# Kernel optimization log

Hardware: AMD Instinct MI355X
Metric: run time of the kernel (lower is better)

The kernel has to match this reference:

```python
import jax, jax.numpy as jnp
from jax import lax
import numpy as np
import math

IN_CH = 256
SCALES = [128, 256, 512]
ASPECT = [0.5, 1.0, 2.0]
NUM_A = len(SCALES) * len(ASPECT)  # 9
PRENMS_TOPK = 2000
RPN_TOPK = 1000
NMS_TH = 0.7
MIN_SIZE = 16.0
IMG_H = IMG_W = 1600
FEAT_H = FEAT_W = 200
BBOX_CLIP = math.log(1000.0 / 16.0)  # standard dw/dh clamp in box decoding


def setup_inputs() -> dict:
    key = jax.random.key(0)
    ks = jax.random.split(key, 6)
    image = jax.random.normal(ks[0], (1, 3, IMG_H, IMG_W), jnp.float32)
    feat = jax.random.normal(ks[1], (1, IN_CH, FEAT_H, FEAT_W), jnp.float32)
    # params init per init_weights(): normal(std=0.01), zero bias
    conv_w = jax.random.normal(ks[2], (IN_CH, IN_CH, 3, 3), jnp.float32) * 0.01
    conv_b = jnp.zeros((IN_CH,), jnp.float32)
    cls_w = jax.random.normal(ks[3], (NUM_A, IN_CH, 1, 1), jnp.float32) * 0.01
    cls_b = jnp.zeros((NUM_A,), jnp.float32)
    reg_w = jax.random.normal(ks[4], (NUM_A * 4, IN_CH, 1, 1), jnp.float32) * 0.01
    reg_b = jnp.zeros((NUM_A * 4,), jnp.float32)
    return dict(image=image, feat=feat, conv_w=conv_w, conv_b=conv_b,
                cls_w=cls_w, cls_b=cls_b, reg_w=reg_w, reg_b=reg_b)


def _conv(x, w, b, pad):
    y = lax.conv_general_dilated(x, w, (1, 1), [(pad, pad), (pad, pad)],
                                 dimension_numbers=('NCHW', 'OIHW', 'NCHW'))
    return y + b[None, :, None, None]


def _generate_anchors(img_hw, feat_hw):
    # static (numpy) anchor grid, faithful to generate_anchors_
    gh, gw = feat_hw
    ih, iw = img_hw
    sh, sw = ih // gh, iw // gw
    scales = np.array(SCALES, np.float32)
    ar = np.array(ASPECT, np.float32)
    hr = np.sqrt(ar)
    wr = 1.0 / hr
    ws = (wr[:, None] * scales[None, :]).reshape(-1)
    hs = (hr[:, None] * scales[None, :]).reshape(-1)
    base = np.round(np.stack([-ws, -hs, ws, hs], axis=1) / 2.0)  # (A,4)
    sx = np.arange(gw, dtype=np.float32) * sw
    sy = np.arange(gh, dtype=np.float32) * sh
    yy, xx = np.meshgrid(sy, sx, indexing='ij')
    xx = xx.reshape(-1)
    yy = yy.reshape(-1)
    shifts = np.stack([xx, yy, xx, yy], axis=1)  # (H*W,4)
    anchors = (shifts[:, None, :] + base[None, :, :]).reshape(-1, 4)
    return jnp.asarray(anchors, jnp.float32)


def _apply_deltas(anchors, deltas):
    w = anchors[:, 2] - anchors[:, 0]
    h = anchors[:, 3] - anchors[:, 1]
    cx = anchors[:, 0] + 0.5 * w
    cy = anchors[:, 1] + 0.5 * h
    dx, dy = deltas[:, 0], deltas[:, 1]
    dw = jnp.minimum(deltas[:, 2], BBOX_CLIP)
    dh = jnp.minimum(deltas[:, 3], BBOX_CLIP)
    pcx = dx * w + cx
    pcy = dy * h + cy
    pw = jnp.exp(dw) * w
    ph = jnp.exp(dh) * h
    return jnp.stack([pcx - 0.5 * pw, pcy - 0.5 * ph,
                      pcx + 0.5 * pw, pcy + 0.5 * ph], axis=1)


def _nms_keep(boxes, valid, thresh):
    # boxes sorted by descending score; greedy NMS via dense IoU matrix
    K = boxes.shape[0]
    area = (boxes[:, 2] - boxes[:, 0]) * (boxes[:, 3] - boxes[:, 1])
    lt = jnp.maximum(boxes[:, None, :2], boxes[None, :, :2])
    rb = jnp.minimum(boxes[:, None, 2:], boxes[None, :, 2:])
    wh = jnp.maximum(rb - lt, 0.0)
    inter = wh[..., 0] * wh[..., 1]
    iou = inter / (area[:, None] + area[None, :] - inter + 1e-9)
    idx = jnp.arange(K)

    def body(i, keep):
        sup = (iou[i] > thresh) & keep[i] & (idx > i)
        return keep & (~sup)

    return lax.fori_loop(0, K, body, valid)


def reference(image, feat, conv_w, conv_b, cls_w, cls_b, reg_w, reg_b):
    H, W = feat.shape[-2], feat.shape[-1]
    x = jax.nn.relu(_conv(feat, conv_w, conv_b, 1))          # (1,C,H,W)
    cls = _conv(x, cls_w, cls_b, 0)                          # (1,A,H,W)
    scores = cls.transpose(0, 2, 3, 1).reshape(-1)           # (H*W*A,)
    reg = _conv(x, reg_w, reg_b, 0)                          # (1,4A,H,W)
    deltas = reg.reshape(1, NUM_A, 4, H, W).transpose(0, 3, 4, 1, 2).reshape(-1, 4)
    anchors = _generate_anchors((image.shape[-2], image.shape[-1]), (H, W))
    proposals = _apply_deltas(anchors, lax.stop_gradient(deltas))  # .detach() in source

    s = jax.nn.sigmoid(scores)
    topv, topi = lax.top_k(s, PRENMS_TOPK)                   # sorted descending
    p = proposals[topi]
    ih = jnp.float32(image.shape[-2])
    iw = jnp.float32(image.shape[-1])
    p = jnp.stack([jnp.clip(p[:, 0], 0.0, iw), jnp.clip(p[:, 1], 0.0, ih),
                   jnp.clip(p[:, 2], 0.0, iw), jnp.clip(p[:, 3], 0.0, ih)], axis=1)
    valid = ((p[:, 2] - p[:, 0]) >= MIN_SIZE) & ((p[:, 3] - p[:, 1]) >= MIN_SIZE)
    sc = jnp.where(valid, topv, -1.0)                        # invalid -> score -1 (masked out)
    order = jnp.argsort(-sc)
    b = p[order]
    sc = sc[order]
    v = valid[order]
    keep = _nms_keep(b, v, NMS_TH)
    final = jnp.where(keep, sc, -1.0)
    fi = jnp.argsort(-final)[:RPN_TOPK]                      # post-NMS sort + topk
    sel = final[fi]
    out_boxes = jnp.where(sel[:, None] > 0.0, b[fi], 0.0)
    out_scores = jnp.where(sel > 0.0, sel, 0.0)
    return out_boxes, out_scores
```

## Files before the change

kernel.cpp:

```cpp
#include <hip/hip_runtime.h>
#include <math.h>

#define FH 200
#define FW 200
#define HW 40000
#define NUM_A 9
#define NANCH 360000
#define PRE_K 2000
#define OUT_K 1000
#define IMG_SZ 1600.0f
#define MIN_SZ 16.0f
#define NMS_TH 0.7f
#define BBOX_CLIP_F 4.135166556742356f

#define OFF_HIST   ((size_t)0)
#define OFF_STATE  ((size_t)1024)
#define OFF_CAND   ((size_t)1088)
#define OFF_BOXS   ((size_t)33856)
#define OFF_SCS    ((size_t)65856)
#define OFF_MASK   ((size_t)73856)
#define OFF_DIAG   ((size_t)585856)
#define OFF_AWH    ((size_t)602240)
#define OFF_AWM    ((size_t)1781888)
#define OFF_AWL    ((size_t)2961536)
#define OFF_HWH    ((size_t)4141184)
#define OFF_HWM    ((size_t)4165760)
#define OFF_HWL    ((size_t)4190336)
#define OFF_LOGIT  ((size_t)4214912)
#define OFF_PH     ((size_t)18614912)
#define OFF_PM     ((size_t)39094912)
#define OFF_PL     ((size_t)59574912)
#define OFF_PROP   ((size_t)18614912)
#define OFF_SCORE  ((size_t)24374912)

typedef __attribute__((ext_vector_type(8))) short short8;
typedef __attribute__((ext_vector_type(4))) float floatx4;
#define MFMA16(a, b, c) __builtin_amdgcn_mfma_f32_16x16x32_bf16(a, b, c, 0, 0, 0)

__device__ __forceinline__ unsigned short rne_bf16(float v) {
  unsigned int bb = __float_as_uint(v);
  return (unsigned short)((bb + 0x7FFFu + ((bb >> 16) & 1u)) >> 16);
}

__device__ __forceinline__ void split3(float v, unsigned short& h,
                                       unsigned short& m, unsigned short& l) {
  h = rne_bf16(v);
  float r1 = v - __uint_as_float(((unsigned int)h) << 16);
  m = rne_bf16(r1);
  float r2 = r1 - __uint_as_float(((unsigned int)m) << 16);
  l = rne_bf16(r2);
}

__global__ __launch_bounds__(256) void prep_all(
    const float* __restrict__ feat, const float* __restrict__ w,
    const float* __restrict__ cls_w, const float* __restrict__ reg_w,
    unsigned short* __restrict__ Ph, unsigned short* __restrict__ Pm,
    unsigned short* __restrict__ Pl, uint4* __restrict__ AW_h,
    uint4* __restrict__ AW_m, uint4* __restrict__ AW_l,
    uint4* __restrict__ HwF_h, uint4* __restrict__ HwF_m,
    uint4* __restrict__ HwF_l) {
  int bx = blockIdx.x;
  int t = threadIdx.x;
  if (bx < 1256) {
    int cib = bx & 7;
    int px = (bx >> 3) * 256 + t;
    if (px >= HW) return;
    unsigned short h[32], m[32], l[32];
#pragma unroll
    for (int ci = 0; ci < 32; ++ci)
      split3(feat[(size_t)(cib * 32 + ci) * HW + px], h[ci], m[ci], l[ci]);
    size_t base = ((size_t)cib * HW + px) * 32;
    uint4* dh = (uint4*)(Ph + base);
    uint4* dm = (uint4*)(Pm + base);
    uint4* dl = (uint4*)(Pl + base);
#pragma unroll
    for (int k = 0; k < 4; ++k) {
      uint4 vh, vm, vl;
      vh.x = h[k * 8 + 0] | (h[k * 8 + 1] << 16);
      vh.y = h[k * 8 + 2] | (h[k * 8 + 3] << 16);
      vh.z = h[k * 8 + 4] | (h[k * 8 + 5] << 16);
      vh.w = h[k * 8 + 6] | (h[k * 8 + 7] << 16);
      vm.x = m[k * 8 + 0] | (m[k * 8 + 1] << 16);
      vm.y = m[k * 8 + 2] | (m[k * 8 + 3] << 16);
      vm.z = m[k * 8 + 4] | (m[k * 8 + 5] << 16);
      vm.w = m[k * 8 + 6] | (m[k * 8 + 7] << 16);
      vl.x = l[k * 8 + 0] | (l[k * 8 + 1] << 16);
      vl.y = l[k * 8 + 2] | (l[k * 8 + 3] << 16);
      vl.z = l[k * 8 + 4] | (l[k * 8 + 5] << 16);
      vl.w = l[k * 8 + 6] | (l[k * 8 + 7] << 16);
      dh[k] = vh; dm[k] = vm; dl[k] = vl;
    }
    return;
  }
  int gid = (bx - 1256) * 256 + t;
  unsigned short h[8], m[8], l[8];
  if (gid < 73728) {
    int L = gid & 63;
    int idx = gid >> 6;
    int cib = idx & 7;
    int tmp = idx >> 3;
    int tap = tmp % 9;
    int ctg = tmp / 9;
    int co = ctg * 16 + (L & 15);
    int ci0 = cib * 32 + (L >> 4) * 8;
#pragma unroll
    for (int j = 0; j < 8; ++j)
      split3(w[(size_t)co * 2304 + (ci0 + j) * 9 + tap], h[j], m[j], l[j]);
    uint4 vh, vm, vl;
    vh.x = h[0] | (h[1] << 16); vh.y = h[2] | (h[3] << 16);
    vh.z = h[4] | (h[5] << 16); vh.w = h[6] | (h[7] << 16);
    vm.x = m[0] | (m[1] << 16); vm.y = m[2] | (m[3] << 16);
    vm.z = m[4] | (m[5] << 16); vm.w = m[6] | (m[7] << 16);
    vl.x = l[0] | (l[1] << 16); vl.y = l[2] | (l[3] << 16);
    vl.z = l[4] | (l[5] << 16); vl.w = l[6] | (l[7] << 16);
    AW_h[gid] = vh; AW_m[gid] = vm; AW_l[gid] = vl;
  } else if (gid < 73728 + 1536) {
    int g2 = gid - 73728;
    int L = g2 & 63;
    int idx = g2 >> 6;
    int kb = idx & 7;
    int mt = idx >> 3;
    int mm = mt * 16 + (L & 15);
    int co0 = kb * 32 + (L >> 4) * 8;
#pragma unroll
    for (int j = 0; j < 8; ++j) {
      float v = 0.f;
      if (mm < 9) v = cls_w[mm * 256 + co0 + j];
      else if (mm < 45) v = reg_w[(mm - 9) * 256 + co0 + j];
      split3(v, h[j], m[j], l[j]);
    }
    uint4 vh, vm, vl;
    vh.x = h[0] | (h[1] << 16); vh.y = h[2] | (h[3] << 16);
    vh.z = h[4] | (h[5] << 16); vh.w = h[6] | (h[7] << 16);
    vm.x = m[0] | (m[1] << 16); vm.y = m[2] | (m[3] << 16);
    vm.z = m[4] | (m[5] << 16); vm.w = m[6] | (m[7] << 16);
    vl.x = l[0] | (l[1] << 16); vl.y = l[2] | (l[3] << 16);
    vl.z = l[4] | (l[5] << 16); vl.w = l[6] | (l[7] << 16);
    HwF_h[g2] = vh; HwF_m[g2] = vm; HwF_l[g2] = vl;
  }
}

__global__ __launch_bounds__(256) void conv_mfma(
    const unsigned short* __restrict__ Ph, const unsigned short* __restrict__ Pm,
    const unsigned short* __restrict__ Pl, const uint4* __restrict__ AW_h,
    const uint4* __restrict__ AW_m, const uint4* __restrict__ AW_l,
    const uint4* __restrict__ HwF_h, const uint4* __restrict__ HwF_m,
    const uint4* __restrict__ HwF_l, const float* __restrict__ bias,
    float* __restrict__ logits) {
  __shared__ alignas(16) unsigned short smem[26112];
  const int t = threadIdx.x;
  const int L = t & 63, wv = t >> 6;
  const int q = L >> 4, nl = L & 15;
  const int w0 = blockIdx.x * 16;
  const int h0 = blockIdx.y * 8;
  const int cb = blockIdx.z;

  floatx4 acc[2][8];
#pragma unroll
  for (int ct = 0; ct < 2; ++ct)
#pragma unroll
    for (int r = 0; r < 8; ++r) acc[ct][r] = (floatx4)0.f;

  unsigned short* flh = smem;
  unsigned short* flm = smem + 7200;
  unsigned short* fll = smem + 14400;

  for (int cib = 0; cib < 8; ++cib) {
    __syncthreads();
#pragma unroll
    for (int j = 0; j < 9; ++j) {
      const int p = j / 3;
      const int c = (j % 3) * 256 + t;
      if (c < 720) {
        int rr = (int)((unsigned)c / 72u);
        int rem = c - rr * 72;
        int cc = rem >> 2, q16 = rem & 3;
        int gr = h0 - 1 + rr, gc = w0 - 1 + cc;
        uint4 v; v.x = v.y = v.z = v.w = 0u;
        if ((unsigned)gr < (unsigned)FH && (unsigned)gc < (unsigned)FW) {
          const unsigned short* pp = (p == 0) ? Ph : (p == 1) ? Pm : Pl;
          v = *(const uint4*)(pp +
                ((size_t)(cib * HW + gr * FW + gc) * 32 + q16 * 8));
        }
        *(uint4*)(smem + p * 7200 + rr * 720 + cc * 40 + q16 * 8) = v;
      }
    }
    __syncthreads();
    __builtin_amdgcn_s_setprio(1);
    const int ctg0 = cb * 8 + wv * 2;
    for (int kh = 0; kh < 3; ++kh) {
      for (int kw = 0; kw < 3; ++kw) {
        const int tap = kh * 3 + kw;
        const int abase = ((ctg0 * 9 + tap) * 8 + cib) * 64 + L;
        const int abase1 = abase + 9 * 8 * 64;
        short8 ah0 = ((const short8*)AW_h)[abase];
        short8 am0 = ((const short8*)AW_m)[abase];
        short8 al0 = ((const short8*)AW_l)[abase];
        short8 ah1 = ((const short8*)AW_h)[abase1];
        short8 am1 = ((const short8*)AW_m)[abase1];
        short8 al1 = ((const short8*)AW_l)[abase1];
        const int cbase = (nl + kw) * 40 + q * 8;
#pragma unroll
        for (int r = 0; r < 8; ++r) {
          const int off = (r + kh) * 720 + cbase;
          short8 bh = *(const short8*)(flh + off);
          short8 bm = *(const short8*)(flm + off);
          short8 bl = *(const short8*)(fll + off);
          acc[0][r] = MFMA16(ah0, bh, acc[0][r]);
          acc[0][r] = MFMA16(ah0, bm, acc[0][r]);
          acc[0][r] = MFMA16(am0, bh, acc[0][r]);
          acc[0][r] = MFMA16(ah0, bl, acc[0][r]);
          acc[0][r] = MFMA16(am0, bm, acc[0][r]);
          acc[0][r] = MFMA16(al0, bh, acc[0][r]);
          acc[1][r] = MFMA16(ah1, bh, acc[1][r]);
          acc[1][r] = MFMA16(ah1, bm, acc[1][r]);
          acc[1][r] = MFMA16(am1, bh, acc[1][r]);
          acc[1][r] = MFMA16(ah1, bl, acc[1][r]);
          acc[1][r] = MFMA16(am1, bm, acc[1][r]);
          acc[1][r] = MFMA16(al1, bh, acc[1][r]);
        }
      }
    }
    __builtin_amdgcn_s_setprio(0);
  }

  float bv[2][4];
#pragma unroll
  for (int ct = 0; ct < 2; ++ct)
#pragma unroll
    for (int i = 0; i < 4; ++i)
      bv[ct][i] = bias[cb * 128 + (wv * 2 + ct) * 16 + q * 4 + i];

  unsigned short* xlh = smem;
  unsigned short* xlm = smem + 8704;
  unsigned short* xll = smem + 17408;

  for (int hp = 0; hp < 2; ++hp) {
    __syncthreads();
#pragma unroll
    for (int ct = 0; ct < 2; ++ct) {
#pragma unroll
      for (int rr = 0; rr < 4; ++rr) {
        int r = hp * 4 + rr;
        unsigned short xh[4], xm[4], xl_[4];
#pragma unroll
        for (int i = 0; i < 4; ++i) {
          float xv = fmaxf(acc[ct][r][i] + bv[ct][i], 0.f);
          split3(xv, xh[i], xm[i], xl_[i]);
        }
        int px_l = rr * 16 + nl;
        int co_l = (wv * 2 + ct) * 16 + q * 4;
        uint2 ph, pm, pl;
        ph.x = xh[0] | (xh[1] << 16); ph.y = xh[2] | (xh[3] << 16);
        pm.x = xm[0] | (xm[1] << 16); pm.y = xm[2] | (xm[3] << 16);
        pl.x = xl_[0] | (xl_[1] << 16); pl.y = xl_[2] | (xl_[3] << 16);
        *(uint2*)(xlh + px_l * 136 + co_l) = ph;
        *(uint2*)(xlm + px_l * 136 + co_l) = pm;
        *(uint2*)(xll + px_l * 136 + co_l) = pl;
      }
    }
    __syncthreads();
    floatx4 ha[3];
#pragma unroll
    for (int mt = 0; mt < 3; ++mt) ha[mt] = (floatx4)0.f;
    for (int ks = 0; ks < 4; ++ks) {
      const int off = (wv * 16 + nl) * 136 + ks * 32 + q * 8;
      short8 bh = *(const short8*)(xlh + off);
      short8 bm = *(const short8*)(xlm + off);
      short8 bl = *(const short8*)(xll + off);
#pragma unroll
      for (int mt = 0; mt < 3; ++mt) {
        const int hb = (mt * 8 + cb * 4 + ks) * 64 + L;
        short8 hh = ((const short8*)HwF_h)[hb];
        short8 hm = ((const short8*)HwF_m)[hb];
        short8 hl = ((const short8*)HwF_l)[hb];
        ha[mt] = MFMA16(hh, bh, ha[mt]);
        ha[mt] = MFMA16(hh, bm, ha[mt]);
        ha[mt] = MFMA16(hm, bh, ha[mt]);
        ha[mt] = MFMA16(hh, bl, ha[mt]);
        ha[mt] = MFMA16(hm, bm, ha[mt]);
        ha[mt] = MFMA16(hl, bh, ha[mt]);
      }
    }
    int gr = h0 + hp * 4 + wv;
    int gc = w0 + nl;
    if (gc < FW) {
      float* lp = logits + ((size_t)cb * HW + (size_t)(gr * FW + gc)) * 45;
#pragma unroll
      for (int mt = 0; mt < 3; ++mt)
#pragma unroll
        for (int i = 0; i < 4; ++i) {
          int head = mt * 16 + q * 4 + i;
          if (head < 45) lp[head] = ha[mt][i];
        }
    }
  }
}

__global__ __launch_bounds__(256) void finalize_kernel(
    const float* __restrict__ logits, const float* __restrict__ cls_b,
    const float* __restrict__ reg_b, float* __restrict__ prop,
    float* __restrict__ score, unsigned int* __restrict__ hist) {
  __shared__ unsigned int hsh[256];
  int t = threadIdx.x;
  hsh[t] = 0u;
  __syncthreads();
  int px = blockIdx.x * 256 + t;
  if (px < HW) {
    float A[45];
    const float* lpA = logits + (size_t)px * 45;
    const float* lpB = logits + (size_t)HW * 45 + (size_t)px * 45;
#pragma unroll
    for (int i = 0; i < 45; ++i) A[i] = lpA[i] + lpB[i];
    const float scv[3] = {128.f, 256.f, 512.f};
    const float arv[3] = {0.5f, 1.f, 2.f};
    float sx = (float)(px % FW) * 8.0f;
    float sy = (float)(px / FW) * 8.0f;
#pragma unroll
    for (int a = 0; a < NUM_A; ++a) {
      int ai = a / 3, si = a % 3;
      float hr = sqrtf(arv[ai]);
      float wr = 1.0f / hr;
      float rw = nearbyintf(wr * scv[si] * 0.5f);
      float rh = nearbyintf(hr * scv[si] * 0.5f);
      float ax0 = sx - rw, ay0 = sy - rh, ax1 = sx + rw, ay1 = sy + rh;
      float aw = ax1 - ax0, ah = ay1 - ay0;
      float cx = ax0 + 0.5f * aw, cy = ay0 + 0.5f * ah;
      float dx = A[9 + a * 4 + 0] + reg_b[a * 4 + 0];
      float dy = A[9 + a * 4 + 1] + reg_b[a * 4 + 1];
      float dw = fminf(A[9 + a * 4 + 2] + reg_b[a * 4 + 2], BBOX_CLIP_F);
      float dh = fminf(A[9 + a * 4 + 3] + reg_b[a * 4 + 3], BBOX_CLIP_F);
      float pcx = dx * aw + cx;
      float pcy = dy * ah + cy;
      float pw = expf(dw) * aw;
      float ph = expf(dh) * ah;
      size_t base = (size_t)(px * NUM_A + a) * 4;
      prop[base + 0] = pcx - 0.5f * pw;
      prop[base + 1] = pcy - 0.5f * ph;
      prop[base + 2] = pcx + 0.5f * pw;
      prop[base + 3] = pcy + 0.5f * ph;
      float lg = A[a] + cls_b[a];
      float sv = 1.0f / (1.0f + expf(-lg));
      score[px * NUM_A + a] = sv;
      atomicAdd(&hsh[__float_as_uint(sv) >> 24], 1u);
    }
  }
  __syncthreads();
  if (hsh[t]) atomicAdd(&hist[t], hsh[t]);
}

__global__ __launch_bounds__(256) void hist_kernel(
    const float* __restrict__ score, unsigned int* __restrict__ hist,
    const unsigned int* __restrict__ state, int pass) {
  __shared__ unsigned int h[256];
  int t = threadIdx.x;
  h[t] = 0;
  __syncthreads();
  unsigned int prefix = state[0];
  int shift = 24 - 8 * pass;
  for (int i = blockIdx.x * 256 + t; i < NANCH; i += gridDim.x * 256) {
    unsigned int key = __float_as_uint(score[i]);
    bool m = ((key >> (32 - 8 * pass)) == prefix);
    if (m) atomicAdd(&h[(key >> shift) & 255u], 1u);
  }
  __syncthreads();
  if (h[t]) atomicAdd(&hist[t], h[t]);
}

__global__ __launch_bounds__(256) void scan_kernel(
    unsigned int* __restrict__ hist, unsigned int* __restrict__ state, int pass) {
  __shared__ unsigned int s0[256], s1[256];
  int t = threadIdx.x;
  unsigned int hv = hist[t];
  hist[t] = 0u;
  s0[t] = hv;
  __syncthreads();
  unsigned int* A = s0;
  unsigned int* B = s1;
  for (int off = 1; off < 256; off <<= 1) {
    B[t] = A[t] + ((t + off < 256) ? A[t + off] : 0u);
    __syncthreads();
    unsigned int* tmp = A; A = B; B = tmp;
  }
  unsigned int prefix = (pass == 0) ? 0u : state[0];
  unsigned int rem = (pass == 0) ? (unsigned)PRE_K : state[1];
  unsigned int suf = A[t];
  unsigned int sufn = (t < 255) ? A[t + 1] : 0u;
  if (suf >= rem && sufn < rem) {
    state[0] = (prefix << 8) | (unsigned int)t;
    state[1] = rem - sufn;
  }
}

__global__ __launch_bounds__(256) void collect_kernel(
    const float* __restrict__ score, unsigned int* __restrict__ state,
    unsigned long long* __restrict__ cand) {
  unsigned int T = state[0];
  for (int i = blockIdx.x * 256 + threadIdx.x; i < NANCH; i += gridDim.x * 256) {
    unsigned int key = __float_as_uint(score[i]);
    if (key >= T) {
      unsigned int pos = atomicAdd(&state[4], 1u);
      if (pos < 4096u)
        cand[pos] = ((unsigned long long)key << 32) |
                    (unsigned long long)(~(unsigned int)i);
    }
  }
}

__global__ __launch_bounds__(1024) void sort_gather(
    const unsigned long long* __restrict__ cand,
    const unsigned int* __restrict__ state, const float* __restrict__ prop,
    const float* __restrict__ score, float* __restrict__ boxes_s,
    float* __restrict__ sc_s) {
  __shared__ unsigned long long sk[4096];
  int t = threadIdx.x;
  unsigned int cnt = state[4];
  if (cnt > 4096u) cnt = 4096u;
  for (int e = t; e < 4096; e += 1024) sk[e] = (e < (int)cnt) ? cand[e] : 0ull;
  __syncthreads();
  for (int k = 2; k <= 4096; k <<= 1) {
    for (int j = k >> 1; j > 0; j >>= 1) {
      for (int i = t; i < 4096; i += 1024) {
        int l = i ^ j;
        if (l > i) {
          unsigned long long a = sk[i], bb = sk[l];
          bool up = ((i & k) == 0);
          bool sw = up ? (a < bb) : (a > bb);
          if (sw) { sk[i] = bb; sk[l] = a; }
        }
      }
      __syncthreads();
    }
  }
  float bx[2][4];
  float sc2[2] = {-1.f, -1.f};
  bool valid2[2] = {false, false};
#pragma unroll
  for (int s = 0; s < 2; ++s) {
    int i = t + s * 1024;
    bx[s][0] = bx[s][1] = bx[s][2] = bx[s][3] = 0.f;
    if (i < PRE_K) {
      unsigned long long v = sk[i];
      unsigned int idx = ~(unsigned int)(v & 0xFFFFFFFFull);
      float4 p = *(const float4*)(prop + (size_t)idx * 4);
      float x0 = fminf(fmaxf(p.x, 0.f), IMG_SZ);
      float y0 = fminf(fmaxf(p.y, 0.f), IMG_SZ);
      float x1 = fminf(fmaxf(p.z, 0.f), IMG_SZ);
      float y1 = fminf(fmaxf(p.w, 0.f), IMG_SZ);
      bool valid = (x1 - x0 >= MIN_SZ) && (y1 - y0 >= MIN_SZ);
      bx[s][0] = x0; bx[s][1] = y0; bx[s][2] = x1; bx[s][3] = y1;
      valid2[s] = valid;
      sc2[s] = valid ? score[idx] : -1.0f;
    }
  }
  __syncthreads();
  int* A = (int*)sk;
  int* B = A + 2048;
#pragma unroll
  for (int s = 0; s < 2; ++s) {
    int i = t + s * 1024;
    A[i] = (i < PRE_K && valid2[s]) ? 1 : 0;
  }
  __syncthreads();
  for (int off = 1; off < 2048; off <<= 1) {
#pragma unroll
    for (int s = 0; s < 2; ++s) {
      int i = t + s * 1024;
      B[i] = A[i] + ((i >= off) ? A[i - off] : 0);
    }
    __syncthreads();
    int* tmp = A; A = B; B = tmp;
  }
  int total = A[2047];
#pragma unroll
  for (int s = 0; s < 2; ++s) {
    int i = t + s * 1024;
    if (i < PRE_K) {
      int inc = A[i];
      int pos = valid2[s] ? (inc - 1) : (total + (i - inc));
      boxes_s[pos * 4 + 0] = bx[s][0];
      boxes_s[pos * 4 + 1] = bx[s][1];
      boxes_s[pos * 4 + 2] = bx[s][2];
      boxes_s[pos * 4 + 3] = bx[s][3];
      sc_s[pos] = sc2[s];
    }
  }
}

__global__ __launch_bounds__(64) void iou_kernel(
    const float* __restrict__ boxes_s, unsigned long long* __restrict__ mask,
    unsigned long long* __restrict__ diag) {
  int bi = blockIdx.y, bj = blockIdx.x;
  int t = threadIdx.x;
  __shared__ float4 cb[64];
  int jc = bj * 64 + t;
  float4 z; z.x = z.y = z.z = z.w = 0.f;
  cb[t] = (jc < PRE_K) ? *(const float4*)(boxes_s + (size_t)jc * 4) : z;
  __syncthreads();
  int i = bi * 64 + t;
  if (i >= PRE_K) return;
  float4 a = *(const float4*)(boxes_s + (size_t)i * 4);
  float areaA = (a.z - a.x) * (a.w - a.y);
  unsigned long long bits = 0ull;
  for (int jj = 0; jj < 64; ++jj) {
    int j = bj * 64 + jj;
    if (j < PRE_K && j > i) {
      float4 b = cb[jj];
      float areaB = (b.z - b.x) * (b.w - b.y);
      float ltx = fmaxf(a.x, b.x), lty = fmaxf(a.y, b.y);
      float rbx = fminf(a.z, b.z), rby = fminf(a.w, b.w);
      float w = fmaxf(rbx - ltx, 0.f), h = fmaxf(rby - lty, 0.f);
      float inter = w * h;
      float iou = inter / (areaA + areaB - inter + 1e-9f);
      if (iou > NMS_TH) bits |= (1ull << jj);
    }
  }
  mask[(size_t)i * 32 + bj] = bits;
  if (bi == bj) diag[i] = bits;
}

__global__ __launch_bounds__(256) void nms_out_kernel(
    const float* __restrict__ boxes_s, const float* __restrict__ sc_s,
    const unsigned long long* __restrict__ mask,
    const unsigned long long* __restrict__ diag, float* __restrict__ out) {
  int t = threadIdx.x;
  for (int e = t; e < (OUT_K * 4 + OUT_K); e += 256) out[e] = 0.f;
  __shared__ unsigned long long keepw[32];
  if (t < 64) {
    unsigned long long removed = 0ull;
    if (t < 32) {
      keepw[t] = 0ull;
#pragma unroll
      for (int k = 0; k < 64; ++k) {
        int idx = t * 64 + k;
        if (idx >= PRE_K || sc_s[idx] < 0.f) removed |= (1ull << k);
      }
    }
    const int w = t & 31;
    const int half = t >> 5;
    unsigned int kept = 0;
    for (int b = 0; b < 32; ++b) {
      unsigned long long d = diag[b * 64 + t];
      unsigned long long dead = __shfl(removed, b);
      unsigned long long alive = 0ull;
#pragma unroll
      for (int k = 0; k < 64; ++k) {
        unsigned long long dk = __shfl(d, k);
        if (!((dead >> k) & 1ull)) {
          alive |= (1ull << k);
          dead |= dk;
        }
      }
      if (t == 0) keepw[b] = alive;
      kept += (unsigned)__popcll(alive);
      if (kept >= (unsigned)OUT_K || b == 31) break;
      unsigned long long am = alive;
      const long long rb = (long long)b * 64;
      while (am) {
        int k0 = __ffsll(am) - 1; am &= am - 1;
        int k1 = k0, k2 = k0, k3 = k0, k4 = k0, k5 = k0, k6 = k0, k7 = k0;
        if (am) { k1 = __ffsll(am) - 1; am &= am - 1; }
        if (am) { k2 = __ffsll(am) - 1; am &= am - 1; }
        if (am) { k3 = __ffsll(am) - 1; am &= am - 1; }
        if (am) { k4 = __ffsll(am) - 1; am &= am - 1; }
        if (am) { k5 = __ffsll(am) - 1; am &= am - 1; }
        if (am) { k6 = __ffsll(am) - 1; am &= am - 1; }
        if (am) { k7 = __ffsll(am) - 1; am &= am - 1; }
        unsigned long long v0 = mask[(size_t)(rb + (half ? k1 : k0)) * 32 + w];
        unsigned long long v1 = mask[(size_t)(rb + (half ? k3 : k2)) * 32 + w];
        unsigned long long v2 = mask[(size_t)(rb + (half ? k5 : k4)) * 32 + w];
        unsigned long long v3 = mask[(size_t)(rb + (half ? k7 : k6)) * 32 + w];
        unsigned long long vv = v0 | v1 | v2 | v3;
        unsigned long long hv = __shfl(vv, w + 32);
        if (t < 32) removed |= vv | hv;
      }
    }
  }
  __syncthreads();
  __shared__ unsigned int wbase[32];
  if (t == 0) {
    unsigned int s = 0;
    for (int k = 0; k < 32; ++k) {
      wbase[k] = s;
      s += (unsigned)__popcll(keepw[k]);
    }
  }
  __syncthreads();
  for (int i = t; i < PRE_K; i += 256) {
    unsigned long long w2 = keepw[i >> 6];
    if ((w2 >> (i & 63)) & 1ull) {
      unsigned int pos =
          wbase[i >> 6] +
          (unsigned)__popcll(w2 & ((1ull << (i & 63)) - 1ull));
      if (pos < OUT_K) {
        out[pos * 4 + 0] = boxes_s[i * 4 + 0];
        out[pos * 4 + 1] = boxes_s[i * 4 + 1];
        out[pos * 4 + 2] = boxes_s[i * 4 + 2];
        out[pos * 4 + 3] = boxes_s[i * 4 + 3];
        out[OUT_K * 4 + pos] = sc_s[i];
      }
    }
  }
}

extern "C" void kernel_launch(void* const* d_in, const int* in_sizes, int n_in,
                              void* d_out, int out_size, void* d_ws,
                              size_t ws_size, hipStream_t stream) {
  const float* feat = (const float*)d_in[1];
  const float* convw = (const float*)d_in[2];
  const float* convb = (const float*)d_in[3];
  const float* clsw = (const float*)d_in[4];
  const float* clsb = (const float*)d_in[5];
  const float* regw = (const float*)d_in[6];
  const float* regb = (const float*)d_in[7];

  char* ws = (char*)d_ws;
  unsigned int* hist = (unsigned int*)(ws + OFF_HIST);
  unsigned int* state = (unsigned int*)(ws + OFF_STATE);
  unsigned long long* cand = (unsigned long long*)(ws + OFF_CAND);
  float* boxes_s = (float*)(ws + OFF_BOXS);
  float* sc_s = (float*)(ws + OFF_SCS);
  unsigned long long* mask = (unsigned long long*)(ws + OFF_MASK);
  unsigned long long* diag = (unsigned long long*)(ws + OFF_DIAG);
  uint4* AW_h = (uint4*)(ws + OFF_AWH);
  uint4* AW_m = (uint4*)(ws + OFF_AWM);
  uint4* AW_l = (uint4*)(ws + OFF_AWL);
  uint4* HwF_h = (uint4*)(ws + OFF_HWH);
  uint4* HwF_m = (uint4*)(ws + OFF_HWM);
  uint4* HwF_l = (uint4*)(ws + OFF_HWL);
  float* logits = (float*)(ws + OFF_LOGIT);
  unsigned short* Ph = (unsigned short*)(ws + OFF_PH);
  unsigned short* Pm = (unsigned short*)(ws + OFF_PM);
  unsigned short* Pl = (unsigned short*)(ws + OFF_PL);
  float* prop = (float*)(ws + OFF_PROP);
  float* score = (float*)(ws + OFF_SCORE);
  float* out = (float*)d_out;

  hipMemsetAsync(ws, 0, OFF_STATE + 64, stream);

  prep_all<<<1550, 256, 0, stream>>>(feat, convw, clsw, regw, Ph, Pm, Pl,
                                     AW_h, AW_m, AW_l, HwF_h, HwF_m, HwF_l);
  conv_mfma<<<dim3(13, 25, 2), 256, 0, stream>>>(Ph, Pm, Pl, AW_h, AW_m, AW_l,
                                                 HwF_h, HwF_m, HwF_l, convb,
                                                 logits);
  finalize_kernel<<<157, 256, 0, stream>>>(logits, clsb, regb, prop, score,
                                           hist);
  scan_kernel<<<1, 256, 0, stream>>>(hist, state, 0);
  for (int p = 1; p < 4; ++p) {
    hist_kernel<<<256, 256, 0, stream>>>(score, hist, state, p);
    scan_kernel<<<1, 256, 0, stream>>>(hist, state, p);
  }
  collect_kernel<<<256, 256, 0, stream>>>(score, state, cand);
  sort_gather<<<1, 1024, 0, stream>>>(cand, state, prop, score, boxes_s, sc_s);
  iou_kernel<<<dim3(32, 32), 64, 0, stream>>>(boxes_s, mask, diag);
  nms_out_kernel<<<1, 256, 0, stream>>>(boxes_s, sc_s, mask, diag, out);
}
```

Baseline: 635.9 us.

## Fuse post-conv selection pipeline into persistent kernels with grid barriers

Merges finalize, the four radix-select histogram/scan passes, candidate collection and the sort/gather into one 40-block persistent kernel that uses atomic grid barriers in place of kernel boundaries. It also folds IoU mask computation and NMS output into a single kernel where the last-finishing block runs the serial NMS, and sets an occupancy hint on the conv kernel. The aim is to remove roughly a dozen small kernel launches and their gaps. The cost is spin-wait barriers, which rely on all 40 blocks being co-resident, and less parallelism in the finalize stage.

```diff
diff --git a/kernel.cpp b/kernel.cpp
--- a/kernel.cpp
+++ b/kernel.cpp
@@ -14,24 +14,25 @@
 #define BBOX_CLIP_F 4.135166556742356f
 
 #define OFF_HIST   ((size_t)0)
-#define OFF_STATE  ((size_t)1024)
-#define OFF_CAND   ((size_t)1088)
-#define OFF_BOXS   ((size_t)33856)
-#define OFF_SCS    ((size_t)65856)
-#define OFF_MASK   ((size_t)73856)
-#define OFF_DIAG   ((size_t)585856)
-#define OFF_AWH    ((size_t)602240)
-#define OFF_AWM    ((size_t)1781888)
-#define OFF_AWL    ((size_t)2961536)
-#define OFF_HWH    ((size_t)4141184)
-#define OFF_HWM    ((size_t)4165760)
-#define OFF_HWL    ((size_t)4190336)
-#define OFF_LOGIT  ((size_t)4214912)
-#define OFF_PH     ((size_t)18614912)
-#define OFF_PM     ((size_t)39094912)
-#define OFF_PL     ((size_t)59574912)
-#define OFF_PROP   ((size_t)18614912)
-#define OFF_SCORE  ((size_t)24374912)
+#define OFF_STATE  ((size_t)4096)
+#define OFF_BAR    ((size_t)4160)
+#define OFF_CAND   ((size_t)4224)
+#define OFF_BOXS   ((size_t)36992)
+#define OFF_SCS    ((size_t)68992)
+#define OFF_MASK   ((size_t)76992)
+#define OFF_DIAG   ((size_t)588992)
+#define OFF_AWH    ((size_t)605376)
+#define OFF_AWM    ((size_t)1785024)
+#define OFF_AWL    ((size_t)2964672)
+#define OFF_HWH    ((size_t)4144320)
+#define OFF_HWM    ((size_t)4168896)
+#define OFF_HWL    ((size_t)4193472)
+#define OFF_LOGIT  ((size_t)4218048)
+#define OFF_PH     ((size_t)18618048)
+#define OFF_PM     ((size_t)39098048)
+#define OFF_PL     ((size_t)59578048)
+#define OFF_PROP   ((size_t)18618048)
+#define OFF_SCORE  ((size_t)24378048)
 
 typedef __attribute__((ext_vector_type(8))) short short8;
 typedef __attribute__((ext_vector_type(4))) float floatx4;
@@ -49,6 +50,17 @@
   m = rne_bf16(r1);
   float r2 = r1 - __uint_as_float(((unsigned int)m) << 16);
   l = rne_bf16(r2);
+}
+
+__device__ __forceinline__ void grid_bar(unsigned int* cnt, unsigned int target) {
+  __syncthreads();
+  if (threadIdx.x == 0) {
+    __threadfence();
+    atomicAdd(cnt, 1u);
+    while (atomicAdd(cnt, 0u) < target) __builtin_amdgcn_s_sleep(16);
+  }
+  __syncthreads();
+  __threadfence();
 }
 
 __global__ __launch_bounds__(256) void prep_all(
@@ -140,7 +152,7 @@
   }
 }
 
-__global__ __launch_bounds__(256) void conv_mfma(
+__global__ __launch_bounds__(256, 3) void conv_mfma(
     const unsigned short* __restrict__ Ph, const unsigned short* __restrict__ Pm,
     const unsigned short* __restrict__ Pl, const uint4* __restrict__ AW_h,
     const uint4* __restrict__ AW_m, const uint4* __restrict__ AW_l,
@@ -297,15 +309,23 @@
   }
 }
 
-__global__ __launch_bounds__(256) void finalize_kernel(
+__global__ __launch_bounds__(1024) void postproc1(
     const float* __restrict__ logits, const float* __restrict__ cls_b,
     const float* __restrict__ reg_b, float* __restrict__ prop,
-    float* __restrict__ score, unsigned int* __restrict__ hist) {
-  __shared__ unsigned int hsh[256];
-  int t = threadIdx.x;
-  hsh[t] = 0u;
-  __syncthreads();
-  int px = blockIdx.x * 256 + t;
+    float* __restrict__ score, unsigned int* __restrict__ hist,
+    unsigned int* __restrict__ state, unsigned long long* __restrict__ cand,
+    unsigned int* __restrict__ barcnt, float* __restrict__ boxes_s,
+    float* __restrict__ sc_s) {
+  __shared__ unsigned long long sk[4096];
+  __shared__ unsigned int bc[2];
+  unsigned int* hsh = (unsigned int*)sk;
+  unsigned int* s0 = (unsigned int*)sk + 256;
+  unsigned int* s1 = (unsigned int*)sk + 512;
+  const int t = threadIdx.x;
+  const unsigned int nb = gridDim.x;
+  if (t < 256) hsh[t] = 0u;
+  __syncthreads();
+  int px = blockIdx.x * 1024 + t;
   if (px < HW) {
     float A[45];
     const float* lpA = logits + (size_t)px * 45;
@@ -346,57 +366,47 @@
     }
   }
   __syncthreads();
-  if (hsh[t]) atomicAdd(&hist[t], hsh[t]);
-}
-
-__global__ __launch_bounds__(256) void hist_kernel(
-    const float* __restrict__ score, unsigned int* __restrict__ hist,
-    const unsigned int* __restrict__ state, int pass) {
-  __shared__ unsigned int h[256];
-  int t = threadIdx.x;
-  h[t] = 0;
-  __syncthreads();
-  unsigned int prefix = state[0];
-  int shift = 24 - 8 * pass;
-  for (int i = blockIdx.x * 256 + t; i < NANCH; i += gridDim.x * 256) {
-    unsigned int key = __float_as_uint(score[i]);
-    bool m = ((key >> (32 - 8 * pass)) == prefix);
-    if (m) atomicAdd(&h[(key >> shift) & 255u], 1u);
-  }
-  __syncthreads();
-  if (h[t]) atomicAdd(&hist[t], h[t]);
-}
-
-__global__ __launch_bounds__(256) void scan_kernel(
-    unsigned int* __restrict__ hist, unsigned int* __restrict__ state, int pass) {
-  __shared__ unsigned int s0[256], s1[256];
-  int t = threadIdx.x;
-  unsigned int hv = hist[t];
-  hist[t] = 0u;
-  s0[t] = hv;
-  __syncthreads();
-  unsigned int* A = s0;
-  unsigned int* B = s1;
-  for (int off = 1; off < 256; off <<= 1) {
-    B[t] = A[t] + ((t + off < 256) ? A[t + off] : 0u);
-    __syncthreads();
-    unsigned int* tmp = A; A = B; B = tmp;
-  }
-  unsigned int prefix = (pass == 0) ? 0u : state[0];
-  unsigned int rem = (pass == 0) ? (unsigned)PRE_K : state[1];
-  unsigned int suf = A[t];
-  unsigned int sufn = (t < 255) ? A[t + 1] : 0u;
-  if (suf >= rem && sufn < rem) {
-    state[0] = (prefix << 8) | (unsigned int)t;
-    state[1] = rem - sufn;
-  }
-}
-
-__global__ __launch_bounds__(256) void collect_kernel(
-    const float* __restrict__ score, unsigned int* __restrict__ state,
-    unsigned long long* __restrict__ cand) {
-  unsigned int T = state[0];
-  for (int i = blockIdx.x * 256 + threadIdx.x; i < NANCH; i += gridDim.x * 256) {
+  if (t < 256 && hsh[t]) atomicAdd(&hist[t], hsh[t]);
+  grid_bar(barcnt, nb);
+  unsigned int prefix = 0u, rem = (unsigned int)PRE_K;
+  for (int pass = 0; pass < 4; ++pass) {
+    if (t < 256) s0[t] = hist[pass * 256 + t];
+    __syncthreads();
+    unsigned int* A = s0;
+    unsigned int* B = s1;
+    for (int off = 1; off < 256; off <<= 1) {
+      if (t < 256) B[t] = A[t] + ((t + off < 256) ? A[t + off] : 0u);
+      __syncthreads();
+      unsigned int* tmp = A; A = B; B = tmp;
+    }
+    if (t < 256) {
+      unsigned int suf = A[t];
+      unsigned int sufn = (t < 255) ? A[t + 1] : 0u;
+      if (suf >= rem && sufn < rem) {
+        bc[0] = (prefix << 8) | (unsigned int)t;
+        bc[1] = rem - sufn;
+      }
+    }
+    __syncthreads();
+    prefix = bc[0];
+    rem = bc[1];
+    __syncthreads();
+    if (pass < 3) {
+      if (t < 256) hsh[t] = 0u;
+      __syncthreads();
+      const int shift = 24 - 8 * (pass + 1);
+      const int fsh = 32 - 8 * (pass + 1);
+      for (int i = blockIdx.x * 1024 + t; i < NANCH; i += nb * 1024) {
+        unsigned int key = __float_as_uint(score[i]);
+        if ((key >> fsh) == prefix) atomicAdd(&hsh[(key >> shift) & 255u], 1u);
+      }
+      __syncthreads();
+      if (t < 256 && hsh[t]) atomicAdd(&hist[(pass + 1) * 256 + t], hsh[t]);
+      grid_bar(barcnt, nb * (unsigned)(pass + 2));
+    }
+  }
+  const unsigned int T = prefix;
+  for (int i = blockIdx.x * 1024 + t; i < NANCH; i += nb * 1024) {
     unsigned int key = __float_as_uint(score[i]);
     if (key >= T) {
       unsigned int pos = atomicAdd(&state[4], 1u);
@@ -405,15 +415,8 @@
                     (unsigned long long)(~(unsigned int)i);
     }
   }
-}
-
-__global__ __launch_bounds__(1024) void sort_gather(
-    const unsigned long long* __restrict__ cand,
-    const unsigned int* __restrict__ state, const float* __restrict__ prop,
-    const float* __restrict__ score, float* __restrict__ boxes_s,
-    float* __restrict__ sc_s) {
-  __shared__ unsigned long long sk[4096];
-  int t = threadIdx.x;
+  grid_bar(barcnt, nb * 5u);
+  if (blockIdx.x != 0) return;
   unsigned int cnt = state[4];
   if (cnt > 4096u) cnt = 4096u;
   for (int e = t; e < 4096; e += 1024) sk[e] = (e < (int)cnt) ? cand[e] : 0ull;
@@ -454,29 +457,29 @@
     }
   }
   __syncthreads();
-  int* A = (int*)sk;
-  int* B = A + 2048;
+  int* Ai = (int*)sk;
+  int* Bi = Ai + 2048;
 #pragma unroll
   for (int s = 0; s < 2; ++s) {
     int i = t + s * 1024;
-    A[i] = (i < PRE_K && valid2[s]) ? 1 : 0;
+    Ai[i] = (i < PRE_K && valid2[s]) ? 1 : 0;
   }
   __syncthreads();
   for (int off = 1; off < 2048; off <<= 1) {
 #pragma unroll
     for (int s = 0; s < 2; ++s) {
       int i = t + s * 1024;
-      B[i] = A[i] + ((i >= off) ? A[i - off] : 0);
-    }
-    __syncthreads();
-    int* tmp = A; A = B; B = tmp;
-  }
-  int total = A[2047];
+      Bi[i] = Ai[i] + ((i >= off) ? Ai[i - off] : 0);
+    }
+    __syncthreads();
+    int* tmp = Ai; Ai = Bi; Bi = tmp;
+  }
+  int total = Ai[2047];
 #pragma unroll
   for (int s = 0; s < 2; ++s) {
     int i = t + s * 1024;
     if (i < PRE_K) {
-      int inc = A[i];
+      int inc = Ai[i];
       int pos = valid2[s] ? (inc - 1) : (total + (i - inc));
       boxes_s[pos * 4 + 0] = bx[s][0];
       boxes_s[pos * 4 + 1] = bx[s][1];
@@ -487,45 +490,55 @@
   }
 }
 
-__global__ __launch_bounds__(64) void iou_kernel(
-    const float* __restrict__ boxes_s, unsigned long long* __restrict__ mask,
-    unsigned long long* __restrict__ diag) {
-  int bi = blockIdx.y, bj = blockIdx.x;
-  int t = threadIdx.x;
-  __shared__ float4 cb[64];
-  int jc = bj * 64 + t;
-  float4 z; z.x = z.y = z.z = z.w = 0.f;
-  cb[t] = (jc < PRE_K) ? *(const float4*)(boxes_s + (size_t)jc * 4) : z;
-  __syncthreads();
-  int i = bi * 64 + t;
-  if (i >= PRE_K) return;
-  float4 a = *(const float4*)(boxes_s + (size_t)i * 4);
-  float areaA = (a.z - a.x) * (a.w - a.y);
-  unsigned long long bits = 0ull;
-  for (int jj = 0; jj < 64; ++jj) {
-    int j = bj * 64 + jj;
-    if (j < PRE_K && j > i) {
-      float4 b = cb[jj];
-      float areaB = (b.z - b.x) * (b.w - b.y);
-      float ltx = fmaxf(a.x, b.x), lty = fmaxf(a.y, b.y);
-      float rbx = fminf(a.z, b.z), rby = fminf(a.w, b.w);
-      float w = fmaxf(rbx - ltx, 0.f), h = fmaxf(rby - lty, 0.f);
-      float inter = w * h;
-      float iou = inter / (areaA + areaB - inter + 1e-9f);
-      if (iou > NMS_TH) bits |= (1ull << jj);
-    }
-  }
-  mask[(size_t)i * 32 + bj] = bits;
-  if (bi == bj) diag[i] = bits;
-}
-
-__global__ __launch_bounds__(256) void nms_out_kernel(
+__global__ __launch_bounds__(256) void iou_nms(
     const float* __restrict__ boxes_s, const float* __restrict__ sc_s,
-    const unsigned long long* __restrict__ mask,
-    const unsigned long long* __restrict__ diag, float* __restrict__ out) {
-  int t = threadIdx.x;
+    unsigned long long* __restrict__ mask,
+    unsigned long long* __restrict__ diag, unsigned int* __restrict__ done,
+    float* __restrict__ out) {
+  __shared__ float4 cbw[4][64];
+  __shared__ int lastflag;
+  __shared__ unsigned long long keepw[32];
+  __shared__ unsigned int wbase[32];
+  const int t = threadIdx.x;
+  const int wvi = t >> 6, lane = t & 63;
+  const int bj = blockIdx.x * 4 + wvi;
+  const int bi = blockIdx.y;
+  {
+    int jc = bj * 64 + lane;
+    float4 z; z.x = z.y = z.z = z.w = 0.f;
+    cbw[wvi][lane] = (jc < PRE_K) ? *(const float4*)(boxes_s + (size_t)jc * 4) : z;
+  }
+  __syncthreads();
+  int i = bi * 64 + lane;
+  if (i < PRE_K) {
+    float4 a = *(const float4*)(boxes_s + (size_t)i * 4);
+    float areaA = (a.z - a.x) * (a.w - a.y);
+    unsigned long long bits = 0ull;
+    for (int jj = 0; jj < 64; ++jj) {
+      int j = bj * 64 + jj;
+      if (j < PRE_K && j > i) {
+        float4 b = cbw[wvi][jj];
+        float areaB = (b.z - b.x) * (b.w - b.y);
+        float ltx = fmaxf(a.x, b.x), lty = fmaxf(a.y, b.y);
+        float rbx = fminf(a.z, b.z), rby = fminf(a.w, b.w);
+        float w = fmaxf(rbx - ltx, 0.f), h = fmaxf(rby - lty, 0.f);
+        float inter = w * h;
+        float iou = inter / (areaA + areaB - inter + 1e-9f);
+        if (iou > NMS_TH) bits |= (1ull << jj);
+      }
+    }
+    mask[(size_t)i * 32 + bj] = bits;
+    if (bi == bj) diag[i] = bits;
+  }
+  __syncthreads();
+  if (t == 0) {
+    __threadfence();
+    lastflag = (atomicAdd(done, 1u) == gridDim.x * gridDim.y - 1u) ? 1 : 0;
+  }
+  __syncthreads();
+  if (!lastflag) return;
+  __threadfence();
   for (int e = t; e < (OUT_K * 4 + OUT_K); e += 256) out[e] = 0.f;
-  __shared__ unsigned long long keepw[32];
   if (t < 64) {
     unsigned long long removed = 0ull;
     if (t < 32) {
@@ -577,7 +590,6 @@
     }
   }
   __syncthreads();
-  __shared__ unsigned int wbase[32];
   if (t == 0) {
     unsigned int s = 0;
     for (int k = 0; k < 32; ++k) {
@@ -586,18 +598,18 @@
     }
   }
   __syncthreads();
-  for (int i = t; i < PRE_K; i += 256) {
-    unsigned long long w2 = keepw[i >> 6];
-    if ((w2 >> (i & 63)) & 1ull) {
+  for (int i2 = t; i2 < PRE_K; i2 += 256) {
+    unsigned long long w2 = keepw[i2 >> 6];
+    if ((w2 >> (i2 & 63)) & 1ull) {
       unsigned int pos =
-          wbase[i >> 6] +
-          (unsigned)__popcll(w2 & ((1ull << (i & 63)) - 1ull));
+          wbase[i2 >> 6] +
+          (unsigned)__popcll(w2 & ((1ull << (i2 & 63)) - 1ull));
       if (pos < OUT_K) {
-        out[pos * 4 + 0] = boxes_s[i * 4 + 0];
-        out[pos * 4 + 1] = boxes_s[i * 4 + 1];
-        out[pos * 4 + 2] = boxes_s[i * 4 + 2];
-        out[pos * 4 + 3] = boxes_s[i * 4 + 3];
-        out[OUT_K * 4 + pos] = sc_s[i];
+        out[pos * 4 + 0] = boxes_s[i2 * 4 + 0];
+        out[pos * 4 + 1] = boxes_s[i2 * 4 + 1];
+        out[pos * 4 + 2] = boxes_s[i2 * 4 + 2];
+        out[pos * 4 + 3] = boxes_s[i2 * 4 + 3];
+        out[OUT_K * 4 + pos] = sc_s[i2];
       }
     }
   }
@@ -617,6 +629,7 @@
   char* ws = (char*)d_ws;
   unsigned int* hist = (unsigned int*)(ws + OFF_HIST);
   unsigned int* state = (unsigned int*)(ws + OFF_STATE);
+  unsigned int* bar = (unsigned int*)(ws + OFF_BAR);
   unsigned long long* cand = (unsigned long long*)(ws + OFF_CAND);
   float* boxes_s = (float*)(ws + OFF_BOXS);
   float* sc_s = (float*)(ws + OFF_SCS);
@@ -636,22 +649,15 @@
   float* score = (float*)(ws + OFF_SCORE);
   float* out = (float*)d_out;
 
-  hipMemsetAsync(ws, 0, OFF_STATE + 64, stream);
+  hipMemsetAsync(ws, 0, OFF_CAND, stream);
 
   prep_all<<<1550, 256, 0, stream>>>(feat, convw, clsw, regw, Ph, Pm, Pl,
                                      AW_h, AW_m, AW_l, HwF_h, HwF_m, HwF_l);
   conv_mfma<<<dim3(13, 25, 2), 256, 0, stream>>>(Ph, Pm, Pl, AW_h, AW_m, AW_l,
                                                  HwF_h, HwF_m, HwF_l, convb,
                                                  logits);
-  finalize_kernel<<<157, 256, 0, stream>>>(logits, clsb, regb, prop, score,
-                                           hist);
-  scan_kernel<<<1, 256, 0, stream>>>(hist, state, 0);
-  for (int p = 1; p < 4; ++p) {
-    hist_kernel<<<256, 256, 0, stream>>>(score, hist, state, p);
-    scan_kernel<<<1, 256, 0, stream>>>(hist, state, p);
-  }
-  collect_kernel<<<256, 256, 0, stream>>>(score, state, cand);
-  sort_gather<<<1, 1024, 0, stream>>>(cand, state, prop, score, boxes_s, sc_s);
-  iou_kernel<<<dim3(32, 32), 64, 0, stream>>>(boxes_s, mask, diag);
-  nms_out_kernel<<<1, 256, 0, stream>>>(boxes_s, sc_s, mask, diag, out);
-}
+  postproc1<<<40, 1024, 0, stream>>>(logits, clsb, regb, prop, score, hist,
+                                     state, cand, bar, boxes_s, sc_s);
+  iou_nms<<<dim3(8, 32), 256, 0, stream>>>(boxes_s, sc_s, mask, diag, bar + 8,
+                                           out);
+}
```

After: 644.3 us. Within noise of the previous version (+1.3%).

## Prefetch conv input tiles into registers and fuse histogram scans via last-block tickets

Applied to the files above, without the earlier changes.

The conv kernel now loads the next input-channel block's halo tile into registers while the MFMA loop runs on the current shared-memory tile, then stores it after a barrier. This hides global-load latency behind compute, and launch bounds are raised to ask for 3 blocks per CU. The radix-select scan is folded into the tail of the finalize and histogram kernels using an atomic ticket, so the last block does the scan. That removes four single-block kernel launches, at the cost of more register pressure from the 9-entry prefetch buffer and reliance on fence and ticket ordering.

```diff
diff --git a/kernel.cpp b/kernel.cpp
--- a/kernel.cpp
+++ b/kernel.cpp
@@ -140,7 +140,7 @@
   }
 }
 
-__global__ __launch_bounds__(256) void conv_mfma(
+__global__ __launch_bounds__(256, 3) void conv_mfma(
     const unsigned short* __restrict__ Ph, const unsigned short* __restrict__ Pm,
     const unsigned short* __restrict__ Pl, const uint4* __restrict__ AW_h,
     const uint4* __restrict__ AW_m, const uint4* __restrict__ AW_l,
@@ -165,27 +165,51 @@
   unsigned short* flm = smem + 7200;
   unsigned short* fll = smem + 14400;
 
+  uint4 pv[9];
+
+#define PREFETCH(CIB)                                                        \
+  {                                                                          \
+    _Pragma("unroll")                                                        \
+    for (int j = 0; j < 9; ++j) {                                            \
+      const int p = j / 3;                                                   \
+      const int c = (j % 3) * 256 + t;                                       \
+      uint4 v; v.x = v.y = v.z = v.w = 0u;                                   \
+      if (c < 720) {                                                         \
+        int rr = (int)((unsigned)c / 72u);                                   \
+        int rem = c - rr * 72;                                               \
+        int cc = rem >> 2, q16 = rem & 3;                                    \
+        int gr = h0 - 1 + rr, gc = w0 - 1 + cc;                              \
+        if ((unsigned)gr < (unsigned)FH && (unsigned)gc < (unsigned)FW) {    \
+          const unsigned short* pp = (p == 0) ? Ph : (p == 1) ? Pm : Pl;     \
+          v = *(const uint4*)(pp +                                           \
+                ((size_t)((CIB) * HW + gr * FW + gc) * 32 + q16 * 8));       \
+        }                                                                    \
+      }                                                                      \
+      pv[j] = v;                                                             \
+    }                                                                        \
+  }
+
+#define STORE_STAGE()                                                        \
+  {                                                                          \
+    _Pragma("unroll")                                                        \
+    for (int j = 0; j < 9; ++j) {                                            \
+      const int p = j / 3;                                                   \
+      const int c = (j % 3) * 256 + t;                                       \
+      if (c < 720) {                                                         \
+        int rr = (int)((unsigned)c / 72u);                                   \
+        int rem = c - rr * 72;                                               \
+        int cc = rem >> 2, q16 = rem & 3;                                    \
+        *(uint4*)(smem + p * 7200 + rr * 720 + cc * 40 + q16 * 8) = pv[j];   \
+      }                                                                      \
+    }                                                                        \
+  }
+
+  PREFETCH(0);
+  STORE_STAGE();
+  __syncthreads();
+
   for (int cib = 0; cib < 8; ++cib) {
-    __syncthreads();
-#pragma unroll
-    for (int j = 0; j < 9; ++j) {
-      const int p = j / 3;
-      const int c = (j % 3) * 256 + t;
-      if (c < 720) {
-        int rr = (int)((unsigned)c / 72u);
-        int rem = c - rr * 72;
-        int cc = rem >> 2, q16 = rem & 3;
-        int gr = h0 - 1 + rr, gc = w0 - 1 + cc;
-        uint4 v; v.x = v.y = v.z = v.w = 0u;
-        if ((unsigned)gr < (unsigned)FH && (unsigned)gc < (unsigned)FW) {
-          const unsigned short* pp = (p == 0) ? Ph : (p == 1) ? Pm : Pl;
-          v = *(const uint4*)(pp +
-                ((size_t)(cib * HW + gr * FW + gc) * 32 + q16 * 8));
-        }
-        *(uint4*)(smem + p * 7200 + rr * 720 + cc * 40 + q16 * 8) = v;
-      }
-    }
-    __syncthreads();
+    if (cib < 7) PREFETCH(cib + 1);
     __builtin_amdgcn_s_setprio(1);
     const int ctg0 = cb * 8 + wv * 2;
     for (int kh = 0; kh < 3; ++kh) {
@@ -222,7 +246,14 @@
       }
     }
     __builtin_amdgcn_s_setprio(0);
-  }
+    __syncthreads();
+    if (cib < 7) {
+      STORE_STAGE();
+      __syncthreads();
+    }
+  }
+#undef PREFETCH
+#undef STORE_STAGE
 
   float bv[2][4];
 #pragma unroll
@@ -300,8 +331,10 @@
 __global__ __launch_bounds__(256) void finalize_kernel(
     const float* __restrict__ logits, const float* __restrict__ cls_b,
     const float* __restrict__ reg_b, float* __restrict__ prop,
-    float* __restrict__ score, unsigned int* __restrict__ hist) {
-  __shared__ unsigned int hsh[256];
+    float* __restrict__ score, unsigned int* __restrict__ hist,
+    unsigned int* __restrict__ state) {
+  __shared__ unsigned int hsh[256], s1[256];
+  __shared__ int lastb;
   int t = threadIdx.x;
   hsh[t] = 0u;
   __syncthreads();
@@ -347,43 +380,66 @@
   }
   __syncthreads();
   if (hsh[t]) atomicAdd(&hist[t], hsh[t]);
-}
-
-__global__ __launch_bounds__(256) void hist_kernel(
-    const float* __restrict__ score, unsigned int* __restrict__ hist,
-    const unsigned int* __restrict__ state, int pass) {
-  __shared__ unsigned int h[256];
-  int t = threadIdx.x;
-  h[t] = 0;
-  __syncthreads();
-  unsigned int prefix = state[0];
-  int shift = 24 - 8 * pass;
-  for (int i = blockIdx.x * 256 + t; i < NANCH; i += gridDim.x * 256) {
-    unsigned int key = __float_as_uint(score[i]);
-    bool m = ((key >> (32 - 8 * pass)) == prefix);
-    if (m) atomicAdd(&h[(key >> shift) & 255u], 1u);
-  }
-  __syncthreads();
-  if (h[t]) atomicAdd(&hist[t], h[t]);
-}
-
-__global__ __launch_bounds__(256) void scan_kernel(
-    unsigned int* __restrict__ hist, unsigned int* __restrict__ state, int pass) {
-  __shared__ unsigned int s0[256], s1[256];
-  int t = threadIdx.x;
+  __syncthreads();
+  if (t == 0) lastb = (atomicAdd(&state[8], 1u) == gridDim.x - 1u) ? 1 : 0;
+  __syncthreads();
+  if (!lastb) return;
+  __threadfence();
   unsigned int hv = hist[t];
   hist[t] = 0u;
-  s0[t] = hv;
-  __syncthreads();
-  unsigned int* A = s0;
+  hsh[t] = hv;
+  __syncthreads();
+  unsigned int* A = hsh;
   unsigned int* B = s1;
   for (int off = 1; off < 256; off <<= 1) {
     B[t] = A[t] + ((t + off < 256) ? A[t + off] : 0u);
     __syncthreads();
     unsigned int* tmp = A; A = B; B = tmp;
   }
-  unsigned int prefix = (pass == 0) ? 0u : state[0];
-  unsigned int rem = (pass == 0) ? (unsigned)PRE_K : state[1];
+  unsigned int rem = (unsigned)PRE_K;
+  unsigned int suf = A[t];
+  unsigned int sufn = (t < 255) ? A[t + 1] : 0u;
+  if (suf >= rem && sufn < rem) {
+    state[0] = (unsigned int)t;
+    state[1] = rem - sufn;
+  }
+}
+
+__global__ __launch_bounds__(256) void hist_scan_kernel(
+    const float* __restrict__ score, unsigned int* __restrict__ hist,
+    unsigned int* __restrict__ state, unsigned int* __restrict__ ticket,
+    int pass) {
+  __shared__ unsigned int h[256], s1[256];
+  __shared__ int lastb;
+  int t = threadIdx.x;
+  h[t] = 0;
+  __syncthreads();
+  unsigned int prefix = state[0];
+  int shift = 24 - 8 * pass;
+  for (int i = blockIdx.x * 256 + t; i < NANCH; i += gridDim.x * 256) {
+    unsigned int key = __float_as_uint(score[i]);
+    if ((key >> (32 - 8 * pass)) == prefix)
+      atomicAdd(&h[(key >> shift) & 255u], 1u);
+  }
+  __syncthreads();
+  if (h[t]) atomicAdd(&hist[t], h[t]);
+  __syncthreads();
+  if (t == 0) lastb = (atomicAdd(ticket, 1u) == gridDim.x - 1u) ? 1 : 0;
+  __syncthreads();
+  if (!lastb) return;
+  __threadfence();
+  unsigned int hv = hist[t];
+  hist[t] = 0u;
+  h[t] = hv;
+  __syncthreads();
+  unsigned int* A = h;
+  unsigned int* B = s1;
+  for (int off = 1; off < 256; off <<= 1) {
+    B[t] = A[t] + ((t + off < 256) ? A[t + off] : 0u);
+    __syncthreads();
+    unsigned int* tmp = A; A = B; B = tmp;
+  }
+  unsigned int rem = state[1];
   unsigned int suf = A[t];
   unsigned int sufn = (t < 255) ? A[t + 1] : 0u;
   if (suf >= rem && sufn < rem) {
@@ -644,12 +700,10 @@
                                                  HwF_h, HwF_m, HwF_l, convb,
                                                  logits);
   finalize_kernel<<<157, 256, 0, stream>>>(logits, clsb, regb, prop, score,
-                                           hist);
-  scan_kernel<<<1, 256, 0, stream>>>(hist, state, 0);
-  for (int p = 1; p < 4; ++p) {
-    hist_kernel<<<256, 256, 0, stream>>>(score, hist, state, p);
-    scan_kernel<<<1, 256, 0, stream>>>(hist, state, p);
-  }
+                                           hist, state);
+  for (int p = 1; p < 4; ++p)
+    hist_scan_kernel<<<256, 256, 0, stream>>>(score, hist, state,
+                                              &state[8 + p], p);
   collect_kernel<<<256, 256, 0, stream>>>(score, state, cand);
   sort_gather<<<1, 1024, 0, stream>>>(cand, state, prop, score, boxes_s, sc_s);
   iou_kernel<<<dim3(32, 32), 64, 0, stream>>>(boxes_s, mask, diag);
```

After: 615.3 us. 3.2% less time.
